# Kernel tuning notes

Hardware: AMD Instinct MI355X
Metric: run time of the kernel (lower is better)

## Reference

```python
import jax, jax.numpy as jnp
import numpy as np

B, T, F_, H1, H2, HEADS = 64, 128, 64, 32, 64, 4
E = H2 * F_  # embed_dim = hidden_dims[-1] * feats = 4096


def conv2d(x, w, b):
    # x: [b,c,H,W], w: [o,c,kh,kw], SAME padding (kernel 3 -> pad 1)
    y = jax.lax.conv_general_dilated(x, w, (1, 1), 'SAME',
                                     dimension_numbers=('NCHW', 'OIHW', 'NCHW'))
    return y + b[None, :, None, None]


def gru_layer(xs, h0, wg, bg, wc, bc):
    # xs: [b,t,c,H,W]; h0: [b,h,H,W]. Standard ConvGRU cell:
    #   r,u = sigmoid(conv([x,h])); cand = tanh(conv([x, r*h]))
    #   h' = (1-u)*h + u*cand
    def step(h, x):
        g = conv2d(jnp.concatenate([x, h], axis=1), wg, bg)
        r, u = jnp.split(jax.nn.sigmoid(g), 2, axis=1)
        cand = jnp.tanh(conv2d(jnp.concatenate([x, r * h], axis=1), wc, bc))
        h_next = (1.0 - u) * h + u * cand
        return h_next, h_next
    hT, ys = jax.lax.scan(step, h0, jnp.swapaxes(xs, 0, 1))
    return jnp.swapaxes(ys, 0, 1), hT  # [b,t,h,H,W], [b,h,H,W]


def mha(q, k, v, w_qkv, b_qkv, w_out, b_out):
    # q: [b,1,E], k/v: [b,t,E]; torch nn.MultiheadAttention (eval, no dropout)
    wq, wk, wv = jnp.split(w_qkv, 3, axis=0)
    bq, bk, bv = jnp.split(b_qkv, 3, axis=0)
    dh = E // HEADS
    def heads(x, w, bb):
        y = x @ w.T + bb
        b_, l_, _ = y.shape
        return y.reshape(b_, l_, HEADS, dh).transpose(0, 2, 1, 3)  # [b,h,l,dh]
    qh, kh, vh = heads(q, wq, bq), heads(k, wk, bk), heads(v, wv, bv)
    scores = jnp.einsum('bhqd,bhkd->bhqk', qh, kh) / jnp.sqrt(jnp.float32(dh))
    attn = jax.nn.softmax(scores, axis=-1)
    ctx = jnp.einsum('bhqk,bhkd->bhqd', attn, vh)
    ctx = ctx.transpose(0, 2, 1, 3).reshape(q.shape[0], q.shape[1], E)
    return ctx @ w_out.T + b_out


def setup_inputs() -> dict:
    key = jax.random.key(0)
    ks = jax.random.split(key, 24)
    s = 0.05
    d = {'x': jax.random.normal(ks[0], (B, T, F_), dtype=jnp.float32)}
    # encoder layer 0: in=1, h=H1; layer 1: in=H1, h=H2
    d['wg_e0'] = jax.random.normal(ks[1], (2 * H1, 1 + H1, 3, 3)) * s
    d['bg_e0'] = jnp.zeros((2 * H1,))
    d['wc_e0'] = jax.random.normal(ks[2], (H1, 1 + H1, 3, 3)) * s
    d['bc_e0'] = jnp.zeros((H1,))
    d['wg_e1'] = jax.random.normal(ks[3], (2 * H2, H1 + H2, 3, 3)) * s
    d['bg_e1'] = jnp.zeros((2 * H2,))
    d['wc_e1'] = jax.random.normal(ks[4], (H2, H1 + H2, 3, 3)) * s
    d['bc_e1'] = jnp.zeros((H2,))
    # decoder: input dim = 2*H2; hidden dims reversed [H2, H1]
    d['wg_d0'] = jax.random.normal(ks[5], (2 * H2, 2 * H2 + H2, 3, 3)) * s
    d['bg_d0'] = jnp.zeros((2 * H2,))
    d['wc_d0'] = jax.random.normal(ks[6], (H2, 2 * H2 + H2, 3, 3)) * s
    d['bc_d0'] = jnp.zeros((H2,))
    d['wg_d1'] = jax.random.normal(ks[7], (2 * H1, H2 + H1, 3, 3)) * s
    d['bg_d1'] = jnp.zeros((2 * H1,))
    d['wc_d1'] = jax.random.normal(ks[8], (H1, H2 + H1, 3, 3)) * s
    d['bc_d1'] = jnp.zeros((H1,))
    d['w_qkv'] = jax.random.normal(ks[9], (3 * E, E)) * (1.0 / np.sqrt(E))
    d['b_qkv'] = jnp.zeros((3 * E,))
    d['w_out'] = jax.random.normal(ks[10], (E, E)) * (1.0 / np.sqrt(E))
    d['b_out'] = jnp.zeros((E,))
    d['w_fin'] = jax.random.normal(ks[11], (1, H1, 1, 1)) * s
    d['b_fin'] = jnp.zeros((1,))
    return d


def reference(x, wg_e0, bg_e0, wc_e0, bc_e0, wg_e1, bg_e1, wc_e1, bc_e1,
              wg_d0, bg_d0, wc_d0, bc_d0, wg_d1, bg_d1, wc_d1, bc_d1,
              w_qkv, b_qkv, w_out, b_out, w_fin, b_fin):
    b, t, f = x.shape
    xr = x.reshape(b, t, 1, f, 1)
    # encoder (2 ConvGRU layers, zero init states)
    y0, h0 = gru_layer(xr, jnp.zeros((b, H1, f, 1), x.dtype), wg_e0, bg_e0, wc_e0, bc_e0)
    y1, h1 = gru_layer(y0, jnp.zeros((b, H2, f, 1), x.dtype), wg_e1, bg_e1, wc_e1, bc_e1)
    # attention bottleneck: query = last hidden, memory = encoder outputs
    query = h1.reshape(b, 1, E)
    memory = y1.reshape(b, t, E)
    context = mha(query, memory, memory, w_qkv, b_qkv, w_out, b_out)  # [b,1,E]
    ctx = context.reshape(b, 1, H2, f, 1)
    dec_in = jnp.concatenate([y1, jnp.broadcast_to(ctx, (b, t, H2, f, 1))], axis=2)
    # decoder init states: encoder last states reversed -> [h1 (H2), h0 (H1)]
    z0, _ = gru_layer(dec_in, h1, wg_d0, bg_d0, wc_d0, bc_d0)
    z1, _ = gru_layer(z0, h0, wg_d1, bg_d1, wc_d1, bc_d1)  # [b,t,H1,f,1]
    # final 1x1 conv applied per timestep == channel contraction
    rec = jnp.einsum('btcfw,oc->btofw', z1, w_fin[:, :, 0, 0]) + b_fin[None, None, :, None, None]
    return rec.reshape(b, t, f)
```

## Files before the change

kernel.cpp:

```cpp
#include <hip/hip_runtime.h>
#include <cstdint>


#define B_  64
#define T_  128
#define TC  32
#define NCH 4

__device__ __forceinline__ float wsum(float v) {
#pragma unroll
  for (int m = 32; m > 0; m >>= 1) v += __shfl_xor(v, m, 64);
  return v;
}
__device__ __forceinline__ float wmaxr(float v) {
#pragma unroll
  for (int m = 32; m > 0; m >>= 1) v = fmaxf(v, __shfl_xor(v, m, 64));
  return v;
}
__device__ __forceinline__ float sigmoidf_(float x) {
  return 1.f / (1.f + __expf(-x));
}
__device__ __forceinline__ float tanhf_(float x) {
  x = fminf(fmaxf(x, -15.f), 15.f);
  float e2 = __expf(2.f * x);
  return (e2 - 1.f) / (e2 + 1.f);
}

struct PackArgs {
  const float* src[16];
  float* dst[16];
  int intot[16];
  int ic0[16];
  int icn[16];
  int oc[16];
};

__global__ __launch_bounds__(256) void pack_all_kernel(PackArgs pa) {
  const int j = blockIdx.y;
  const int icN = pa.icn[j];
  const int total = pa.oc[j] * icN * 3;
  const int i = blockIdx.x * 256 + threadIdx.x;
  if (i >= total) return;
  const int per_oc = icN * 3;
  const int oc = i / per_oc;
  const int rem = i - oc * per_oc;
  const int ic = rem / 3, dk = rem - ic * 3;
  pa.dst[j][i] =
      pa.src[j][((size_t)(oc * pa.intot[j] + pa.ic0[j] + ic) * 3 + dk) * 3 + 1];
}

template <int INC, int OG, int OCC>
__global__ __launch_bounds__(256) void conv_x_kernel(
    const float* __restrict__ seq, int seqC, size_t sB,
    const float* __restrict__ ctx,
    const float* __restrict__ Wgx, const float* __restrict__ Wcx,
    const float* __restrict__ bg, const float* __restrict__ bc,
    float* __restrict__ out) {
  constexpr int OCT = OG + OCC;
  constexpr int NJ = OG / 32;
  constexpr int NJC = OCC / 32;
  const int btl = blockIdx.x;
  const int b = btl >> 5;
  const int tl = btl & 31;
  const int ocg = threadIdx.x >> 3;
  const int f0 = (threadIdx.x & 7) << 3;
  __shared__ float sin_[INC][72];

  for (int idx = threadIdx.x; idx < INC * 72; idx += 256) {
    int ic = idx / 72, ff = idx - ic * 72;
    float v = 0.f;
    if (ff >= 1 && ff <= 64) {
      int fs = ff - 1;
      v = (ic < seqC)
              ? seq[(size_t)b * sB + (size_t)tl * seqC * 64 + ic * 64 + fs]
              : ctx[((size_t)b * (INC - seqC) + (ic - seqC)) * 64 + fs];
    }
    sin_[ic][ff] = v;
  }
  __syncthreads();

  if constexpr (INC >= 4) {
    {
      float acc[NJ][8];
#pragma unroll
      for (int j = 0; j < NJ; ++j) {
        float bb = bg[ocg + 32 * j];
#pragma unroll
        for (int ff = 0; ff < 8; ++ff) acc[j][ff] = bb;
      }
      for (int ic0 = 0; ic0 < INC; ic0 += 4) {
        float hv[4][10];
#pragma unroll
        for (int q = 0; q < 4; ++q) {
          float4 a4 = *(const float4*)&sin_[ic0 + q][f0];
          float4 b4 = *(const float4*)&sin_[ic0 + q][f0 + 4];
          float2 c2 = *(const float2*)&sin_[ic0 + q][f0 + 8];
          hv[q][0] = a4.x; hv[q][1] = a4.y; hv[q][2] = a4.z; hv[q][3] = a4.w;
          hv[q][4] = b4.x; hv[q][5] = b4.y; hv[q][6] = b4.z; hv[q][7] = b4.w;
          hv[q][8] = c2.x; hv[q][9] = c2.y;
        }
#pragma unroll
        for (int j = 0; j < NJ; ++j) {
          const int oc = ocg + 32 * j;
          const float4* w4 = (const float4*)(Wgx + ((size_t)oc * INC + ic0) * 3);
          float4 wa = w4[0], wb = w4[1], wc4 = w4[2];
          const float wt[12] = {wa.x, wa.y, wa.z, wa.w, wb.x, wb.y, wb.z, wb.w,
                                wc4.x, wc4.y, wc4.z, wc4.w};
#pragma unroll
          for (int q = 0; q < 4; ++q) {
            const float w0 = wt[3 * q], w1 = wt[3 * q + 1], w2 = wt[3 * q + 2];
#pragma unroll
            for (int ff = 0; ff < 8; ++ff)
              acc[j][ff] = fmaf(w0, hv[q][ff], fmaf(w1, hv[q][ff + 1], fmaf(w2, hv[q][ff + 2], acc[j][ff])));
          }
        }
      }
#pragma unroll
      for (int j = 0; j < NJ; ++j) {
        float* dst = out + ((size_t)btl * OCT + ocg + 32 * j) * 64 + f0;
        *(float4*)dst = make_float4(acc[j][0], acc[j][1], acc[j][2], acc[j][3]);
        *(float4*)(dst + 4) = make_float4(acc[j][4], acc[j][5], acc[j][6], acc[j][7]);
      }
    }
    {
      float acc[NJC][8];
#pragma unroll
      for (int j = 0; j < NJC; ++j) {
        float bb = bc[ocg + 32 * j];
#pragma unroll
        for (int ff = 0; ff < 8; ++ff) acc[j][ff] = bb;
      }
      for (int ic0 = 0; ic0 < INC; ic0 += 4) {
        float hv[4][10];
#pragma unroll
        for (int q = 0; q < 4; ++q) {
          float4 a4 = *(const float4*)&sin_[ic0 + q][f0];
          float4 b4 = *(const float4*)&sin_[ic0 + q][f0 + 4];
          float2 c2 = *(const float2*)&sin_[ic0 + q][f0 + 8];
          hv[q][0] = a4.x; hv[q][1] = a4.y; hv[q][2] = a4.z; hv[q][3] = a4.w;
          hv[q][4] = b4.x; hv[q][5] = b4.y; hv[q][6] = b4.z; hv[q][7] = b4.w;
          hv[q][8] = c2.x; hv[q][9] = c2.y;
        }
#pragma unroll
        for (int j = 0; j < NJC; ++j) {
          const int oc = ocg + 32 * j;
          const float4* w4 = (const float4*)(Wcx + ((size_t)oc * INC + ic0) * 3);
          float4 wa = w4[0], wb = w4[1], wc4 = w4[2];
          const float wt[12] = {wa.x, wa.y, wa.z, wa.w, wb.x, wb.y, wb.z, wb.w,
                                wc4.x, wc4.y, wc4.z, wc4.w};
#pragma unroll
          for (int q = 0; q < 4; ++q) {
            const float w0 = wt[3 * q], w1 = wt[3 * q + 1], w2 = wt[3 * q + 2];
#pragma unroll
            for (int ff = 0; ff < 8; ++ff)
              acc[j][ff] = fmaf(w0, hv[q][ff], fmaf(w1, hv[q][ff + 1], fmaf(w2, hv[q][ff + 2], acc[j][ff])));
          }
        }
      }
#pragma unroll
      for (int j = 0; j < NJC; ++j) {
        float* dst = out + ((size_t)btl * OCT + OG + ocg + 32 * j) * 64 + f0;
        *(float4*)dst = make_float4(acc[j][0], acc[j][1], acc[j][2], acc[j][3]);
        *(float4*)(dst + 4) = make_float4(acc[j][4], acc[j][5], acc[j][6], acc[j][7]);
      }
    }
  } else {
    float hv[10];
    {
      float4 a4 = *(const float4*)&sin_[0][f0];
      float4 b4 = *(const float4*)&sin_[0][f0 + 4];
      float2 c2 = *(const float2*)&sin_[0][f0 + 8];
      hv[0] = a4.x; hv[1] = a4.y; hv[2] = a4.z; hv[3] = a4.w;
      hv[4] = b4.x; hv[5] = b4.y; hv[6] = b4.z; hv[7] = b4.w;
      hv[8] = c2.x; hv[9] = c2.y;
    }
#pragma unroll
    for (int j = 0; j < NJ; ++j) {
      const int oc = ocg + 32 * j;
      const float w0 = Wgx[oc * 3], w1 = Wgx[oc * 3 + 1], w2 = Wgx[oc * 3 + 2];
      float acc[8];
#pragma unroll
      for (int ff = 0; ff < 8; ++ff)
        acc[ff] = fmaf(w0, hv[ff], fmaf(w1, hv[ff + 1], fmaf(w2, hv[ff + 2], bg[oc])));
      float* dst = out + ((size_t)btl * OCT + oc) * 64 + f0;
      *(float4*)dst = make_float4(acc[0], acc[1], acc[2], acc[3]);
      *(float4*)(dst + 4) = make_float4(acc[4], acc[5], acc[6], acc[7]);
    }
#pragma unroll
    for (int j = 0; j < NJC; ++j) {
      const int oc = ocg + 32 * j;
      const float w0 = Wcx[oc * 3], w1 = Wcx[oc * 3 + 1], w2 = Wcx[oc * 3 + 2];
      float acc[8];
#pragma unroll
      for (int ff = 0; ff < 8; ++ff)
        acc[ff] = fmaf(w0, hv[ff], fmaf(w1, hv[ff + 1], fmaf(w2, hv[ff + 2], bc[oc])));
      float* dst = out + ((size_t)btl * OCT + OG + oc) * 64 + f0;
      *(float4*)dst = make_float4(acc[0], acc[1], acc[2], acc[3]);
      *(float4*)(dst + 4) = make_float4(acc[4], acc[5], acc[6], acc[7]);
    }
  }
}

template <int HC>
__device__ __forceinline__ void gru_body(
    float* smem,
    const float* __restrict__ A,
    const float* __restrict__ Wgh,
    const float* __restrict__ Wch,
    const float* hinit,
    float* __restrict__ Y, size_t yB,
    float* hfinal, int b) {
  constexpr int NR = HC / 32;
  constexpr int OG = 2 * HC;
  constexpr int OCT = 3 * HC;
  float(*Hs)[68] = (float(*)[68])smem;
  float(*Rs)[68] = (float(*)[68])(smem + HC * 68);
  const int tid = threadIdx.x;
  const int ocg = tid >> 4;
  const int f0 = (tid & 15) << 2;
  const int im = (f0 == 0) ? 0 : f0 - 1;
  const bool lo = (f0 == 0), hi = (f0 == 60);

  float hreg[NR][4];
#pragma unroll
  for (int r = 0; r < NR; ++r) {
    const int oc = ocg + 32 * r;
    const float4 v = *(const float4*)(hinit + ((size_t)b * HC + oc) * 64 + f0);
    hreg[r][0] = v.x; hreg[r][1] = v.y; hreg[r][2] = v.z; hreg[r][3] = v.w;
    *(float4*)&Hs[oc][f0] = v;
  }
  __syncthreads();

  for (int tl = 0; tl < TC; ++tl) {
    const float* Abt = A + ((size_t)b * TC + tl) * (OCT * 64);
    float accr[NR][4], accu[NR][4], accc[NR][4];
#pragma unroll
    for (int r = 0; r < NR; ++r) {
      const int oc = ocg + 32 * r;
      const float4 vr = *(const float4*)(Abt + (size_t)oc * 64 + f0);
      const float4 vu = *(const float4*)(Abt + (size_t)(HC + oc) * 64 + f0);
      const float4 vc = *(const float4*)(Abt + (size_t)(OG + oc) * 64 + f0);
      accr[r][0] = vr.x; accr[r][1] = vr.y; accr[r][2] = vr.z; accr[r][3] = vr.w;
      accu[r][0] = vu.x; accu[r][1] = vu.y; accu[r][2] = vu.z; accu[r][3] = vu.w;
      accc[r][0] = vc.x; accc[r][1] = vc.y; accc[r][2] = vc.z; accc[r][3] = vc.w;
    }
#pragma unroll 2
    for (int hc0 = 0; hc0 < HC; hc0 += 4) {
      float hv[4][6];
#pragma unroll
      for (int q = 0; q < 4; ++q) {
        const float4 h4 = *(const float4*)&Hs[hc0 + q][f0];
        const float lf = Hs[hc0 + q][im];
        const float rt = Hs[hc0 + q][f0 + 4];
        hv[q][0] = lo ? 0.f : lf;
        hv[q][1] = h4.x; hv[q][2] = h4.y; hv[q][3] = h4.z; hv[q][4] = h4.w;
        hv[q][5] = hi ? 0.f : rt;
      }
#pragma unroll
      for (int r = 0; r < NR; ++r) {
        {
          const float4* w4 = (const float4*)(Wgh + ((size_t)(ocg + 32 * r) * HC + hc0) * 3);
          const float4 wa = w4[0], wb = w4[1], wc4 = w4[2];
          const float wt[12] = {wa.x, wa.y, wa.z, wa.w, wb.x, wb.y, wb.z, wb.w,
                                wc4.x, wc4.y, wc4.z, wc4.w};
#pragma unroll
          for (int q = 0; q < 4; ++q) {
            const float w0 = wt[3 * q], w1 = wt[3 * q + 1], w2 = wt[3 * q + 2];
#pragma unroll
            for (int ff = 0; ff < 4; ++ff)
              accr[r][ff] = fmaf(w0, hv[q][ff], fmaf(w1, hv[q][ff + 1], fmaf(w2, hv[q][ff + 2], accr[r][ff])));
          }
        }
        {
          const float4* w4 = (const float4*)(Wgh + ((size_t)(HC + ocg + 32 * r) * HC + hc0) * 3);
          const float4 wa = w4[0], wb = w4[1], wc4 = w4[2];
          const float wt[12] = {wa.x, wa.y, wa.z, wa.w, wb.x, wb.y, wb.z, wb.w,
                                wc4.x, wc4.y, wc4.z, wc4.w};
#pragma unroll
          for (int q = 0; q < 4; ++q) {
            const float w0 = wt[3 * q], w1 = wt[3 * q + 1], w2 = wt[3 * q + 2];
#pragma unroll
            for (int ff = 0; ff < 4; ++ff)
              accu[r][ff] = fmaf(w0, hv[q][ff], fmaf(w1, hv[q][ff + 1], fmaf(w2, hv[q][ff + 2], accu[r][ff])));
          }
        }
      }
    }
    float uu[NR][4];
#pragma unroll
    for (int r = 0; r < NR; ++r) {
      float4 rh;
#pragma unroll
      for (int ff = 0; ff < 4; ++ff) {
        uu[r][ff] = sigmoidf_(accu[r][ff]);
        (&rh.x)[ff] = sigmoidf_(accr[r][ff]) * hreg[r][ff];
      }
      *(float4*)&Rs[ocg + 32 * r][f0] = rh;
    }
    __syncthreads();
#pragma unroll 2
    for (int hc0 = 0; hc0 < HC; hc0 += 4) {
      float hv[4][6];
#pragma unroll
      for (int q = 0; q < 4; ++q) {
        const float4 h4 = *(const float4*)&Rs[hc0 + q][f0];
        const float lf = Rs[hc0 + q][im];
        const float rt = Rs[hc0 + q][f0 + 4];
        hv[q][0] = lo ? 0.f : lf;
        hv[q][1] = h4.x; hv[q][2] = h4.y; hv[q][3] = h4.z; hv[q][4] = h4.w;
        hv[q][5] = hi ? 0.f : rt;
      }
#pragma unroll
      for (int r = 0; r < NR; ++r) {
        const float4* w4 = (const float4*)(Wch + ((size_t)(ocg + 32 * r) * HC + hc0) * 3);
        const float4 wa = w4[0], wb = w4[1], wc4 = w4[2];
        const float wt[12] = {wa.x, wa.y, wa.z, wa.w, wb.x, wb.y, wb.z, wb.w,
                              wc4.x, wc4.y, wc4.z, wc4.w};
#pragma unroll
        for (int q = 0; q < 4; ++q) {
          const float w0 = wt[3 * q], w1 = wt[3 * q + 1], w2 = wt[3 * q + 2];
#pragma unroll
          for (int ff = 0; ff < 4; ++ff)
            accc[r][ff] = fmaf(w0, hv[q][ff], fmaf(w1, hv[q][ff + 1], fmaf(w2, hv[q][ff + 2], accc[r][ff])));
        }
      }
    }
#pragma unroll
    for (int r = 0; r < NR; ++r) {
      const int oc = ocg + 32 * r;
      float4 yv;
#pragma unroll
      for (int ff = 0; ff < 4; ++ff) {
        const float cd = tanhf_(accc[r][ff]);
        const float hn = fmaf(uu[r][ff], cd - hreg[r][ff], hreg[r][ff]);
        hreg[r][ff] = hn;
        (&yv.x)[ff] = hn;
      }
      *(float4*)(Y + (size_t)b * yB + (size_t)tl * (HC * 64) + (size_t)oc * 64 + f0) = yv;
      *(float4*)&Hs[oc][f0] = yv;
    }
    __syncthreads();
  }
#pragma unroll
  for (int r = 0; r < NR; ++r) {
    const int oc = ocg + 32 * r;
    *(float4*)(hfinal + ((size_t)b * HC + oc) * 64 + f0) =
        make_float4(hreg[r][0], hreg[r][1], hreg[r][2], hreg[r][3]);
  }
}

template <int HC>
__global__ __launch_bounds__(512) void gru_rec_kernel(
    const float* __restrict__ A, const float* __restrict__ Wgh,
    const float* __restrict__ Wch, const float* hinit,
    float* __restrict__ Y, size_t yB, float* hfinal) {
  __shared__ float smem[2 * HC * 68];
  gru_body<HC>(smem, A, Wgh, Wch, hinit, Y, yB, hfinal, blockIdx.x);
}

struct GruArgs {
  const float* A;
  const float* Wgh;
  const float* Wch;
  const float* hinit;
  float* Y;
  size_t yB;
  float* hfinal;
};

__global__ __launch_bounds__(512) void gru_fused_kernel(GruArgs g64, GruArgs g32) {
  __shared__ float smem[2 * 64 * 68];
  if (blockIdx.x < 64) {
    gru_body<64>(smem, g64.A, g64.Wgh, g64.Wch, g64.hinit, g64.Y, g64.yB,
                 g64.hfinal, blockIdx.x);
  } else {
    gru_body<32>(smem, g32.A, g32.Wgh, g32.Wch, g32.hinit, g32.Y, g32.yB,
                 g32.hfinal, blockIdx.x - 64);
  }
}

template <bool WT>
__global__ __launch_bounds__(256) void gemm64_kernel(
    const float* __restrict__ W, int wrs,
    const float* __restrict__ X, int xrs,
    float* __restrict__ O, int ors,
    const float* __restrict__ bias, int K,
    int ebh, size_t hsW, size_t hsX, size_t hsO, size_t hsB) {
  int eb = blockIdx.x;
  if (ebh > 0) {
    int h = blockIdx.x / ebh;
    eb = blockIdx.x - h * ebh;
    W += h * hsW; X += h * hsX; O += h * hsO;
    if (bias) bias += h * hsB;
  }
  const int e0 = eb * 64;
  __shared__ float Xs[64][68];
  __shared__ float Ws[64][68];
  const int tb4 = (threadIdx.x & 15) << 2;
  const int te4 = (threadIdx.x >> 4) << 2;
  float acc[4][4] = {};
  for (int k0 = 0; k0 < K; k0 += 64) {
    {
      const int row = threadIdx.x >> 2;
      const int kq = (threadIdx.x & 3) << 4;
      const float* src = X + (size_t)row * xrs + k0 + kq;
#pragma unroll
      for (int q = 0; q < 4; ++q) {
        float4 v = *(const float4*)(src + (q << 2));
        Xs[kq + (q << 2) + 0][row] = v.x;
        Xs[kq + (q << 2) + 1][row] = v.y;
        Xs[kq + (q << 2) + 2][row] = v.z;
        Xs[kq + (q << 2) + 3][row] = v.w;
      }
    }
    if (!WT) {
      const int row = threadIdx.x >> 2;
      const int kq = (threadIdx.x & 3) << 4;
      const float* src = W + (size_t)(e0 + row) * wrs + k0 + kq;
#pragma unroll
      for (int q = 0; q < 4; ++q) {
        float4 v = *(const float4*)(src + (q << 2));
        Ws[kq + (q << 2) + 0][row] = v.x;
        Ws[kq + (q << 2) + 1][row] = v.y;
        Ws[kq + (q << 2) + 2][row] = v.z;
        Ws[kq + (q << 2) + 3][row] = v.w;
      }
    } else {
      const int row = threadIdx.x >> 2;
      const int eq = (threadIdx.x & 3) << 4;
      const float* src = W + (size_t)(k0 + row) * wrs + e0 + eq;
#pragma unroll
      for (int q = 0; q < 4; ++q)
        *(float4*)&Ws[row][eq + (q << 2)] = *(const float4*)(src + (q << 2));
    }
    __syncthreads();
#pragma unroll 8
    for (int k = 0; k < 64; ++k) {
      float4 xv = *(const float4*)&Xs[k][tb4];
      float4 wv4 = *(const float4*)&Ws[k][te4];
      const float xb[4] = {xv.x, xv.y, xv.z, xv.w};
      const float we[4] = {wv4.x, wv4.y, wv4.z, wv4.w};
#pragma unroll
      for (int i = 0; i < 4; ++i)
#pragma unroll
        for (int j = 0; j < 4; ++j) acc[i][j] = fmaf(xb[i], we[j], acc[i][j]);
    }
    __syncthreads();
  }
#pragma unroll
  for (int i = 0; i < 4; ++i)
#pragma unroll
    for (int j = 0; j < 4; ++j) {
      float v = acc[i][j];
      if (bias) v += bias[e0 + te4 + j];
      O[(size_t)(tb4 + i) * ors + e0 + te4 + j] = v;
    }
}

__global__ __launch_bounds__(256) void attn_scores_kernel(
    const float* __restrict__ qkh, const float* __restrict__ mem,
    float* __restrict__ scores) {
  const int b = blockIdx.x >> 4;
  const int tt = blockIdx.x & 15;
  const int h = threadIdx.x >> 6;
  const int lane = threadIdx.x & 63;
  const float4* qk4 = (const float4*)(qkh + ((size_t)b * 4 + h) * 4096);
#pragma unroll 2
  for (int ti = 0; ti < 8; ++ti) {
    const int t = tt * 8 + ti;
    const float4* m4 = (const float4*)(mem + ((size_t)b * 128 + t) * 4096);
    float s = 0.f;
    for (int e = lane; e < 1024; e += 64) {
      float4 q = qk4[e], m = m4[e];
      s = fmaf(q.x, m.x, fmaf(q.y, m.y, fmaf(q.z, m.z, fmaf(q.w, m.w, s))));
    }
    s = wsum(s);
    if (lane == 0) scores[((size_t)b * 4 + h) * 128 + t] = s;
  }
}

__global__ __launch_bounds__(256) void attn_softmax_kernel(
    const float* __restrict__ scores, const float* __restrict__ qbuf,
    const float* __restrict__ bqkv, float* __restrict__ attnp) {
  const int b = blockIdx.x;
  const int h = threadIdx.x >> 6;
  const int lane = threadIdx.x & 63;
  const float4* q4 = (const float4*)(qbuf + (size_t)b * 4096 + h * 1024);
  const float4* k4 = (const float4*)(bqkv + 4096 + h * 1024);
  float qb = 0.f;
#pragma unroll
  for (int d = lane; d < 256; d += 64) {
    float4 q = q4[d], k = k4[d];
    qb = fmaf(q.x, k.x, fmaf(q.y, k.y, fmaf(q.z, k.z, fmaf(q.w, k.w, qb))));
  }
  qb = wsum(qb);
  const float* sc = scores + ((size_t)b * 4 + h) * 128;
  float s0 = (sc[lane] + qb) * 0.03125f;
  float s1 = (sc[lane + 64] + qb) * 0.03125f;
  float mx = wmaxr(fmaxf(s0, s1));
  float e0v = __expf(s0 - mx), e1v = __expf(s1 - mx);
  float inv = 1.f / wsum(e0v + e1v);
  attnp[((size_t)b * 4 + h) * 128 + lane] = e0v * inv;
  attnp[((size_t)b * 4 + h) * 128 + lane + 64] = e1v * inv;
}

__global__ __launch_bounds__(256) void attn_wsum_kernel(
    const float* __restrict__ attnp, const float* __restrict__ mem,
    float* __restrict__ wmem) {
  const int b = blockIdx.x >> 4;
  const int eb = blockIdx.x & 15;
  const int e = eb * 256 + threadIdx.x;
  __shared__ float ap[4][128];
  for (int i = threadIdx.x; i < 512; i += 256)
    ap[i >> 7][i & 127] = attnp[(size_t)b * 512 + i];
  __syncthreads();
  float a0 = 0, a1 = 0, a2 = 0, a3 = 0;
  const float* mb = mem + (size_t)b * 128 * 4096 + e;
#pragma unroll 4
  for (int t = 0; t < 128; ++t) {
    float m = mb[(size_t)t * 4096];
    a0 = fmaf(ap[0][t], m, a0);
    a1 = fmaf(ap[1][t], m, a1);
    a2 = fmaf(ap[2][t], m, a2);
    a3 = fmaf(ap[3][t], m, a3);
  }
  wmem[((size_t)b * 4 + 0) * 4096 + e] = a0;
  wmem[((size_t)b * 4 + 1) * 4096 + e] = a1;
  wmem[((size_t)b * 4 + 2) * 4096 + e] = a2;
  wmem[((size_t)b * 4 + 3) * 4096 + e] = a3;
}

__global__ __launch_bounds__(256) void final_kernel(
    const float* __restrict__ z1c,
    const float* __restrict__ wfin, const float* __restrict__ bfin,
    float* __restrict__ out, int tOff) {
  const int idx = blockIdx.x * 256 + threadIdx.x;
  const int f = idx & 63;
  const int tl = (idx >> 6) & 31;
  const int b = idx >> 11;
  const float* zp = z1c + ((size_t)b * TC + tl) * 2048 + f;
  float a = bfin[0];
#pragma unroll
  for (int c = 0; c < 32; ++c) a = fmaf(wfin[c], zp[c * 64], a);
  out[(size_t)b * 8192 + (size_t)(tOff + tl) * 64 + f] = a;
}

extern "C" void kernel_launch(void* const* d_in, const int* in_sizes, int n_in,
                              void* d_out, int out_size, void* d_ws, size_t ws_size,
                              hipStream_t stream) {
  (void)in_sizes; (void)n_in; (void)out_size;
  const float* x     = (const float*)d_in[0];
  const float* wg_e0 = (const float*)d_in[1];
  const float* bg_e0 = (const float*)d_in[2];
  const float* wc_e0 = (const float*)d_in[3];
  const float* bc_e0 = (const float*)d_in[4];
  const float* wg_e1 = (const float*)d_in[5];
  const float* bg_e1 = (const float*)d_in[6];
  const float* wc_e1 = (const float*)d_in[7];
  const float* bc_e1 = (const float*)d_in[8];
  const float* wg_d0 = (const float*)d_in[9];
  const float* bg_d0 = (const float*)d_in[10];
  const float* wc_d0 = (const float*)d_in[11];
  const float* bc_d0 = (const float*)d_in[12];
  const float* wg_d1 = (const float*)d_in[13];
  const float* bg_d1 = (const float*)d_in[14];
  const float* wc_d1 = (const float*)d_in[15];
  const float* bc_d1 = (const float*)d_in[16];
  const float* w_qkv = (const float*)d_in[17];
  const float* b_qkv = (const float*)d_in[18];
  const float* w_out = (const float*)d_in[19];
  const float* b_out = (const float*)d_in[20];
  const float* w_fin = (const float*)d_in[21];
  const float* b_fin = (const float*)d_in[22];
  float* out = (float*)d_out;

  float* WS = (float*)d_ws;
  size_t off = 0;
  auto alloc = [&](size_t n) { float* p = WS + off; off += (n + 63) & ~(size_t)63; return p; };
  float* Amain = alloc((size_t)B_ * TC * 192 * 64);
  float* A96   = alloc((size_t)B_ * TC * 96 * 64);
  float* Y0c  = alloc((size_t)B_ * TC * 32 * 64);
  float* Y1   = alloc((size_t)B_ * T_ * 64 * 64);
  float* Z0p[2] = {alloc((size_t)B_ * TC * 64 * 64), alloc((size_t)B_ * TC * 64 * 64)};
  float* Z1c  = alloc((size_t)B_ * TC * 32 * 64);
  float* He0p[2] = {alloc((size_t)B_ * 32 * 64), alloc((size_t)B_ * 32 * 64)};
  float* He1p[2] = {alloc((size_t)B_ * 64 * 64), alloc((size_t)B_ * 64 * 64)};
  float* Hd0p[2] = {alloc((size_t)B_ * 64 * 64), alloc((size_t)B_ * 64 * 64)};
  float* Hd1p[2] = {alloc((size_t)B_ * 32 * 64), alloc((size_t)B_ * 32 * 64)};
  float* QBUF = alloc((size_t)B_ * 4096);
  float* QKH  = alloc((size_t)B_ * 4 * 4096);
  float* WMEM = alloc((size_t)B_ * 4 * 4096);
  float* CTXB = alloc((size_t)B_ * 4096);
  float* CTXO = alloc((size_t)B_ * 4096);
  float* SCR  = alloc((size_t)B_ * 4 * 128);
  float* ATTN = alloc((size_t)B_ * 4 * 128);
  float* wgx_e0 = alloc(64 * 1 * 3);    float* wgh_e0 = alloc(64 * 32 * 3);
  float* wcx_e0 = alloc(32 * 1 * 3);    float* wch_e0 = alloc(32 * 32 * 3);
  float* wgx_e1 = alloc(128 * 32 * 3);  float* wgh_e1 = alloc(128 * 64 * 3);
  float* wcx_e1 = alloc(64 * 32 * 3);   float* wch_e1 = alloc(64 * 64 * 3);
  float* wgx_d0 = alloc(128 * 128 * 3); float* wgh_d0 = alloc(128 * 64 * 3);
  float* wcx_d0 = alloc(64 * 128 * 3);  float* wch_d0 = alloc(64 * 64 * 3);
  float* wgx_d1 = alloc(64 * 64 * 3);   float* wgh_d1 = alloc(64 * 32 * 3);
  float* wcx_d1 = alloc(32 * 64 * 3);   float* wch_d1 = alloc(32 * 32 * 3);
  if (ws_size < off * sizeof(float)) return;

  {
    PackArgs pa;
    const float* srcs[16] = {wg_e0, wg_e0, wc_e0, wc_e0, wg_e1, wg_e1, wc_e1, wc_e1,
                             wg_d0, wg_d0, wc_d0, wc_d0, wg_d1, wg_d1, wc_d1, wc_d1};
    float* dsts[16] = {wgx_e0, wgh_e0, wcx_e0, wch_e0, wgx_e1, wgh_e1, wcx_e1, wch_e1,
                       wgx_d0, wgh_d0, wcx_d0, wch_d0, wgx_d1, wgh_d1, wcx_d1, wch_d1};
    int intot[16] = {33, 33, 33, 33, 96, 96, 96, 96, 192, 192, 192, 192, 96, 96, 96, 96};
    int ic0[16]   = {0, 1, 0, 1, 0, 32, 0, 32, 0, 128, 0, 128, 0, 64, 0, 64};
    int icn[16]   = {1, 32, 1, 32, 32, 64, 32, 64, 128, 64, 128, 64, 64, 32, 64, 32};
    int occ[16]   = {64, 64, 32, 32, 128, 128, 64, 64, 128, 128, 64, 64, 64, 64, 32, 32};
    for (int j = 0; j < 16; ++j) {
      pa.src[j] = srcs[j]; pa.dst[j] = dsts[j];
      pa.intot[j] = intot[j]; pa.ic0[j] = ic0[j]; pa.icn[j] = icn[j]; pa.oc[j] = occ[j];
    }
    pack_all_kernel<<<dim3(192, 16), 256, 0, stream>>>(pa);
  }

  hipMemsetAsync(He0p[0], 0, (size_t)B_ * 32 * 64 * 4, stream);
  hipMemsetAsync(He1p[0], 0, (size_t)B_ * 64 * 64 * 4, stream);

  auto conv_e0 = [&](int c) {
    conv_x_kernel<1, 64, 32><<<2048, 256, 0, stream>>>(
        x + (size_t)c * TC * 64, 1, (size_t)T_ * 64, nullptr,
        wgx_e0, wcx_e0, bg_e0, bc_e0, A96);
  };
  auto conv_e1 = [&]() {
    conv_x_kernel<32, 128, 64><<<2048, 256, 0, stream>>>(
        Y0c, 32, (size_t)TC * 32 * 64, nullptr,
        wgx_e1, wcx_e1, bg_e1, bc_e1, Amain);
  };

  conv_e0(0);
  gru_rec_kernel<32><<<64, 512, 0, stream>>>(
      A96, wgh_e0, wch_e0, He0p[0], Y0c, (size_t)TC * 2048, He0p[1]);
  conv_e1();
  for (int c = 0; c < NCH; ++c) {
    GruArgs g64 = {Amain, wgh_e1, wch_e1, He1p[c & 1],
                   Y1 + (size_t)c * TC * 4096, (size_t)T_ * 4096, He1p[(c + 1) & 1]};
    if (c < NCH - 1) {
      conv_e0(c + 1);
      GruArgs g32 = {A96, wgh_e0, wch_e0, He0p[(c + 1) & 1],
                     Y0c, (size_t)TC * 2048, He0p[c & 1]};
      gru_fused_kernel<<<128, 512, 0, stream>>>(g64, g32);
      conv_e1();
    } else {
      gru_rec_kernel<64><<<64, 512, 0, stream>>>(
          g64.A, g64.Wgh, g64.Wch, g64.hinit, g64.Y, g64.yB, g64.hfinal);
    }
  }
  float* He0f = He0p[0];
  float* He1f = He1p[0];

  const float* wq = w_qkv;
  const float* wk = w_qkv + (size_t)4096 * 4096;
  const float* wv = w_qkv + (size_t)8192 * 4096;
  gemm64_kernel<false><<<64, 256, 0, stream>>>(wq, 4096, He1f, 4096, QBUF, 4096,
                                               b_qkv, 4096, 0, 0, 0, 0, 0);
  gemm64_kernel<true><<<256, 256, 0, stream>>>(wk, 4096, QBUF, 4096, QKH, 16384,
                                               nullptr, 1024, 64,
                                               (size_t)1024 * 4096, 1024, 4096, 0);
  attn_scores_kernel<<<B_ * 16, 256, 0, stream>>>(QKH, Y1, SCR);
  attn_softmax_kernel<<<B_, 256, 0, stream>>>(SCR, QBUF, b_qkv, ATTN);
  attn_wsum_kernel<<<B_ * 16, 256, 0, stream>>>(ATTN, Y1, WMEM);
  gemm64_kernel<false><<<64, 256, 0, stream>>>(wv, 4096, WMEM, 16384, CTXB, 4096,
                                               b_qkv + 8192, 4096, 16,
                                               (size_t)1024 * 4096, 4096, 1024, 1024);
  gemm64_kernel<false><<<64, 256, 0, stream>>>(w_out, 4096, CTXB, 4096, CTXO, 4096,
                                               b_out, 4096, 0, 0, 0, 0, 0);

  auto conv_d0 = [&](int c) {
    conv_x_kernel<128, 128, 64><<<2048, 256, 0, stream>>>(
        Y1 + (size_t)c * TC * 4096, 64, (size_t)T_ * 4096, CTXO,
        wgx_d0, wcx_d0, bg_d0, bc_d0, Amain);
  };
  auto conv_d1 = [&](int c) {
    conv_x_kernel<64, 64, 32><<<2048, 256, 0, stream>>>(
        Z0p[c & 1], 64, (size_t)TC * 4096, nullptr,
        wgx_d1, wcx_d1, bg_d1, bc_d1, A96);
  };

  conv_d0(0);
  gru_rec_kernel<64><<<64, 512, 0, stream>>>(
      Amain, wgh_d0, wch_d0, He1f, Z0p[0], (size_t)TC * 4096, Hd0p[1]);
  conv_d1(0);
  for (int c = 1; c < NCH; ++c) {
    conv_d0(c);
    GruArgs g64 = {Amain, wgh_d0, wch_d0, Hd0p[c & 1],
                   Z0p[c & 1], (size_t)TC * 4096, Hd0p[(c + 1) & 1]};
    GruArgs g32 = {A96, wgh_d1, wch_d1,
                   (c - 1 == 0 ? He0f : Hd1p[(c - 1) & 1]),
                   Z1c, (size_t)TC * 2048, Hd1p[c & 1]};
    gru_fused_kernel<<<128, 512, 0, stream>>>(g64, g32);
    final_kernel<<<512, 256, 0, stream>>>(Z1c, w_fin, b_fin, out, (c - 1) * TC);
    conv_d1(c);
  }
  gru_rec_kernel<32><<<64, 512, 0, stream>>>(
      A96, wgh_d1, wch_d1, Hd1p[1], Z1c, (size_t)TC * 2048, Hd1p[0]);
  final_kernel<<<512, 256, 0, stream>>>(Z1c, w_fin, b_fin, out, 3 * TC);
}
```

Before: 8.425 ms.

## Overlap decoder conv and final projection with GRU recurrence in one mega-kernel

Adds a mega_kernel that runs the decoder GRU recurrence blocks alongside independent conv_x input projections and final 1x1 projection tiles for other chunks, selected by block index. Double-buffered activation workspaces (Amp, A96p, Z1p) let the next chunk's convolution proceed while the current recurrence runs. The goal is to fill the GPU, which otherwise sits mostly idle during the 64/128-block sequential GRU kernels, and to cut the number of launches. It needs extra workspace, falls back to the old path when that is not available, and the smem size and 512-thread blocks may reduce occupancy for the conv work.

New measurement: 7.721 ms. 1.09x faster.

```diff
diff --git a/kernel.cpp b/kernel.cpp
--- a/kernel.cpp
+++ b/kernel.cpp
@@ -50,7 +50,8 @@
 }
 
 template <int INC, int OG, int OCC>
-__global__ __launch_bounds__(256) void conv_x_kernel(
+__device__ __forceinline__ void conv_x_body(
+    float (*sin_)[72], int tid, int btl,
     const float* __restrict__ seq, int seqC, size_t sB,
     const float* __restrict__ ctx,
     const float* __restrict__ Wgx, const float* __restrict__ Wcx,
@@ -59,14 +60,12 @@
   constexpr int OCT = OG + OCC;
   constexpr int NJ = OG / 32;
   constexpr int NJC = OCC / 32;
-  const int btl = blockIdx.x;
   const int b = btl >> 5;
   const int tl = btl & 31;
-  const int ocg = threadIdx.x >> 3;
-  const int f0 = (threadIdx.x & 7) << 3;
-  __shared__ float sin_[INC][72];
-
-  for (int idx = threadIdx.x; idx < INC * 72; idx += 256) {
+  const int ocg = tid >> 3;
+  const int f0 = (tid & 7) << 3;
+
+  for (int idx = tid; idx < INC * 72; idx += 256) {
     int ic = idx / 72, ff = idx - ic * 72;
     float v = 0.f;
     if (ff >= 1 && ff <= 64) {
@@ -201,15 +200,46 @@
   }
 }
 
+template <int INC, int OG, int OCC>
+__global__ __launch_bounds__(256) void conv_x_kernel(
+    const float* __restrict__ seq, int seqC, size_t sB,
+    const float* __restrict__ ctx,
+    const float* __restrict__ Wgx, const float* __restrict__ Wcx,
+    const float* __restrict__ bg, const float* __restrict__ bc,
+    float* __restrict__ out) {
+  __shared__ float sin_[INC][72];
+  conv_x_body<INC, OG, OCC>(sin_, threadIdx.x, blockIdx.x, seq, seqC, sB, ctx,
+                            Wgx, Wcx, bg, bc, out);
+}
+
+__device__ __forceinline__ void final_body(
+    int tid, int tile, const float* __restrict__ z1c,
+    const float* __restrict__ wfin, const float* __restrict__ bfin,
+    float* __restrict__ out, int tOff) {
+  const int idx = tile * 256 + tid;
+  const int f = idx & 63;
+  const int tl = (idx >> 6) & 31;
+  const int b = idx >> 11;
+  const float* zp = z1c + ((size_t)b * TC + tl) * 2048 + f;
+  float a = bfin[0];
+#pragma unroll
+  for (int c = 0; c < 32; ++c) a = fmaf(wfin[c], zp[c * 64], a);
+  out[(size_t)b * 8192 + (size_t)(tOff + tl) * 64 + f] = a;
+}
+
+__global__ __launch_bounds__(256) void final_kernel(
+    const float* __restrict__ z1c,
+    const float* __restrict__ wfin, const float* __restrict__ bfin,
+    float* __restrict__ out, int tOff) {
+  final_body(threadIdx.x, blockIdx.x, z1c, wfin, bfin, out, tOff);
+}
+
 template <int HC>
 __device__ __forceinline__ void gru_body(
     float* smem,
-    const float* __restrict__ A,
-    const float* __restrict__ Wgh,
-    const float* __restrict__ Wch,
-    const float* hinit,
-    float* __restrict__ Y, size_t yB,
-    float* hfinal, int b) {
+    const float* __restrict__ A, const float* __restrict__ Wgh,
+    const float* __restrict__ Wch, const float* hinit,
+    float* __restrict__ Y, size_t yB, float* hfinal, int b) {
   constexpr int NR = HC / 32;
   constexpr int OG = 2 * HC;
   constexpr int OCT = 3 * HC;
@@ -376,6 +406,67 @@
   } else {
     gru_body<32>(smem, g32.A, g32.Wgh, g32.Wch, g32.hinit, g32.Y, g32.yB,
                  g32.hfinal, blockIdx.x - 64);
+  }
+}
+
+struct ConvJob {
+  int kind;
+  int nblk;
+  const float* seq;
+  int seqC;
+  size_t sB;
+  const float* ctx;
+  const float* w0;
+  const float* w1;
+  const float* b0;
+  const float* b1;
+  float* out;
+  int tOff;
+};
+
+struct MegaArgs {
+  GruArgs g64;
+  GruArgs g32;
+  int ng64, ng32, njobs;
+  ConvJob jobs[4];
+};
+
+__global__ __launch_bounds__(512) void mega_kernel(MegaArgs ma) {
+  __shared__ float smem[18432];
+  int bid = blockIdx.x;
+  if (bid < ma.ng64) {
+    gru_body<64>(smem, ma.g64.A, ma.g64.Wgh, ma.g64.Wch, ma.g64.hinit,
+                 ma.g64.Y, ma.g64.yB, ma.g64.hfinal, bid);
+    return;
+  }
+  bid -= ma.ng64;
+  if (bid < ma.ng32) {
+    gru_body<32>(smem, ma.g32.A, ma.g32.Wgh, ma.g32.Wch, ma.g32.hinit,
+                 ma.g32.Y, ma.g32.yB, ma.g32.hfinal, bid);
+    return;
+  }
+  bid -= ma.ng32;
+  const int half = threadIdx.x >> 8;
+  const int tid = threadIdx.x & 255;
+#pragma unroll 1
+  for (int j = 0; j < ma.njobs; ++j) {
+    if (bid < ma.jobs[j].nblk) {
+      const ConvJob cj = ma.jobs[j];
+      const int tile = bid * 2 + half;
+      if (cj.kind == 2) {
+        conv_x_body<128, 128, 64>((float(*)[72])(smem + half * 128 * 72), tid,
+                                  tile, cj.seq, cj.seqC, cj.sB, cj.ctx, cj.w0,
+                                  cj.w1, cj.b0, cj.b1, cj.out);
+      } else if (cj.kind == 3) {
+        conv_x_body<64, 64, 32>((float(*)[72])(smem + half * 64 * 72), tid,
+                                tile, cj.seq, cj.seqC, cj.sB, cj.ctx, cj.w0,
+                                cj.w1, cj.b0, cj.b1, cj.out);
+      } else {
+        final_body(tid, tile, cj.seq, cj.w0, cj.b0, cj.out, cj.tOff);
+      }
+      return;
+    }
+    bid -= ma.jobs[j].nblk;
   }
 }
 
@@ -528,21 +619,6 @@
   wmem[((size_t)b * 4 + 1) * 4096 + e] = a1;
   wmem[((size_t)b * 4 + 2) * 4096 + e] = a2;
   wmem[((size_t)b * 4 + 3) * 4096 + e] = a3;
-}
-
-__global__ __launch_bounds__(256) void final_kernel(
-    const float* __restrict__ z1c,
-    const float* __restrict__ wfin, const float* __restrict__ bfin,
-    float* __restrict__ out, int tOff) {
-  const int idx = blockIdx.x * 256 + threadIdx.x;
-  const int f = idx & 63;
-  const int tl = (idx >> 6) & 31;
-  const int b = idx >> 11;
-  const float* zp = z1c + ((size_t)b * TC + tl) * 2048 + f;
-  float a = bfin[0];
-#pragma unroll
-  for (int c = 0; c < 32; ++c) a = fmaf(wfin[c], zp[c * 64], a);
-  out[(size_t)b * 8192 + (size_t)(tOff + tl) * 64 + f] = a;
 }
 
 extern "C" void kernel_launch(void* const* d_in, const int* in_sizes, int n_in,
@@ -577,12 +653,12 @@
   float* WS = (float*)d_ws;
   size_t off = 0;
   auto alloc = [&](size_t n) { float* p = WS + off; off += (n + 63) & ~(size_t)63; return p; };
-  float* Amain = alloc((size_t)B_ * TC * 192 * 64);
-  float* A96   = alloc((size_t)B_ * TC * 96 * 64);
+  float* Amp0 = alloc((size_t)B_ * TC * 192 * 64);
+  float* A960 = alloc((size_t)B_ * TC * 96 * 64);
   float* Y0c  = alloc((size_t)B_ * TC * 32 * 64);
   float* Y1   = alloc((size_t)B_ * T_ * 64 * 64);
   float* Z0p[2] = {alloc((size_t)B_ * TC * 64 * 64), alloc((size_t)B_ * TC * 64 * 64)};
-  float* Z1c  = alloc((size_t)B_ * TC * 32 * 64);
+  float* Z1p0 = alloc((size_t)B_ * TC * 32 * 64);
   float* He0p[2] = {alloc((size_t)B_ * 32 * 64), alloc((size_t)B_ * 32 * 64)};
   float* He1p[2] = {alloc((size_t)B_ * 64 * 64), alloc((size_t)B_ * 64 * 64)};
   float* Hd0p[2] = {alloc((size_t)B_ * 64 * 64), alloc((size_t)B_ * 64 * 64)};
@@ -602,7 +678,17 @@
   float* wcx_d0 = alloc(64 * 128 * 3);  float* wch_d0 = alloc(64 * 64 * 3);
   float* wgx_d1 = alloc(64 * 64 * 3);   float* wgh_d1 = alloc(64 * 32 * 3);
   float* wcx_d1 = alloc(32 * 64 * 3);   float* wch_d1 = alloc(32 * 32 * 3);
-  if (ws_size < off * sizeof(float)) return;
+  const size_t off_r9 = off;
+  float* Amp1 = alloc((size_t)B_ * TC * 192 * 64);
+  float* A961 = alloc((size_t)B_ * TC * 96 * 64);
+  float* Z1p1 = alloc((size_t)B_ * TC * 32 * 64);
+  const size_t off_full = off;
+  if (ws_size < off_r9 * sizeof(float)) return;
+  const bool mega_ok = (ws_size >= off_full * sizeof(float));
+
+  float* Amp[2] = {Amp0, Amp1};
+  float* A96p[2] = {A960, A961};
+  float* Z1p[2] = {Z1p0, Z1p1};
 
   {
     PackArgs pa;
@@ -627,24 +713,24 @@
   auto conv_e0 = [&](int c) {
     conv_x_kernel<1, 64, 32><<<2048, 256, 0, stream>>>(
         x + (size_t)c * TC * 64, 1, (size_t)T_ * 64, nullptr,
-        wgx_e0, wcx_e0, bg_e0, bc_e0, A96);
+        wgx_e0, wcx_e0, bg_e0, bc_e0, A96p[0]);
   };
   auto conv_e1 = [&]() {
     conv_x_kernel<32, 128, 64><<<2048, 256, 0, stream>>>(
         Y0c, 32, (size_t)TC * 32 * 64, nullptr,
-        wgx_e1, wcx_e1, bg_e1, bc_e1, Amain);
+        wgx_e1, wcx_e1, bg_e1, bc_e1, Amp[0]);
   };
 
   conv_e0(0);
   gru_rec_kernel<32><<<64, 512, 0, stream>>>(
-      A96, wgh_e0, wch_e0, He0p[0], Y0c, (size_t)TC * 2048, He0p[1]);
+      A96p[0], wgh_e0, wch_e0, He0p[0], Y0c, (size_t)TC * 2048, He0p[1]);
   conv_e1();
   for (int c = 0; c < NCH; ++c) {
-    GruArgs g64 = {Amain, wgh_e1, wch_e1, He1p[c & 1],
+    GruArgs g64 = {Amp[0], wgh_e1, wch_e1, He1p[c & 1],
                    Y1 + (size_t)c * TC * 4096, (size_t)T_ * 4096, He1p[(c + 1) & 1]};
     if (c < NCH - 1) {
       conv_e0(c + 1);
-      GruArgs g32 = {A96, wgh_e0, wch_e0, He0p[(c + 1) & 1],
+      GruArgs g32 = {A96p[0], wgh_e0, wch_e0, He0p[(c + 1) & 1],
                      Y0c, (size_t)TC * 2048, He0p[c & 1]};
       gru_fused_kernel<<<128, 512, 0, stream>>>(g64, g32);
       conv_e1();
@@ -673,33 +759,88 @@
   gemm64_kernel<false><<<64, 256, 0, stream>>>(w_out, 4096, CTXB, 4096, CTXO, 4096,
                                                b_out, 4096, 0, 0, 0, 0, 0);
 
-  auto conv_d0 = [&](int c) {
+  if (mega_ok) {
+    auto JD0 = [&](int c, float* dst) {
+      ConvJob j{}; j.kind = 2; j.nblk = 1024;
+      j.seq = Y1 + (size_t)c * TC * 4096; j.seqC = 64; j.sB = (size_t)T_ * 4096;
+      j.ctx = CTXO; j.w0 = wgx_d0; j.w1 = wcx_d0; j.b0 = bg_d0; j.b1 = bc_d0;
+      j.out = dst; return j;
+    };
+    auto JD1 = [&](float* z0src, float* dst) {
+      ConvJob j{}; j.kind = 3; j.nblk = 1024;
+      j.seq = z0src; j.seqC = 64; j.sB = (size_t)TC * 4096;
+      j.ctx = nullptr; j.w0 = wgx_d1; j.w1 = wcx_d1; j.b0 = bg_d1; j.b1 = bc_d1;
+      j.out = dst; return j;
+    };
+    auto JFIN = [&](float* z1src, int tOff) {
+      ConvJob j{}; j.kind = 4; j.nblk = 256;
+      j.seq = z1src; j.w0 = w_fin; j.b0 = b_fin; j.out = out; j.tOff = tOff;
+      return j;
+    };
+    auto mega = [&](const GruArgs* a64, const GruArgs* a32, int nj,
+                    const ConvJob* js) {
+      MegaArgs ma{};
+      ma.ng64 = a64 ? 64 : 0; if (a64) ma.g64 = *a64;
+      ma.ng32 = a32 ? 64 : 0; if (a32) ma.g32 = *a32;
+      ma.njobs = nj;
+      int grid = ma.ng64 + ma.ng32;
+      for (int i = 0; i < nj; ++i) { ma.jobs[i] = js[i]; grid += js[i].nblk; }
+      mega_kernel<<<grid, 512, 0, stream>>>(ma);
+    };
+
+    GruArgs gd0[4], gd1[4];
+    for (int c = 0; c < 4; ++c) {
+      gd0[c] = {Amp[c & 1], wgh_d0, wch_d0,
+                (c == 0 ? He1f : Hd0p[c & 1]),
+                Z0p[c & 1], (size_t)TC * 4096, Hd0p[(c + 1) & 1]};
+      gd1[c] = {A96p[c & 1], wgh_d1, wch_d1,
+                (c == 0 ? He0f : Hd1p[c & 1]),
+                Z1p[c & 1], (size_t)TC * 2048, Hd1p[(c + 1) & 1]};
+    }
+
     conv_x_kernel<128, 128, 64><<<2048, 256, 0, stream>>>(
-        Y1 + (size_t)c * TC * 4096, 64, (size_t)T_ * 4096, CTXO,
-        wgx_d0, wcx_d0, bg_d0, bc_d0, Amain);
-  };
-  auto conv_d1 = [&](int c) {
-    conv_x_kernel<64, 64, 32><<<2048, 256, 0, stream>>>(
-        Z0p[c & 1], 64, (size_t)TC * 4096, nullptr,
-        wgx_d1, wcx_d1, bg_d1, bc_d1, A96);
-  };
-
-  conv_d0(0);
-  gru_rec_kernel<64><<<64, 512, 0, stream>>>(
-      Amain, wgh_d0, wch_d0, He1f, Z0p[0], (size_t)TC * 4096, Hd0p[1]);
-  conv_d1(0);
-  for (int c = 1; c < NCH; ++c) {
-    conv_d0(c);
-    GruArgs g64 = {Amain, wgh_d0, wch_d0, Hd0p[c & 1],
-                   Z0p[c & 1], (size_t)TC * 4096, Hd0p[(c + 1) & 1]};
-    GruArgs g32 = {A96, wgh_d1, wch_d1,
-                   (c - 1 == 0 ? He0f : Hd1p[(c - 1) & 1]),
-                   Z1c, (size_t)TC * 2048, Hd1p[c & 1]};
-    gru_fused_kernel<<<128, 512, 0, stream>>>(g64, g32);
-    final_kernel<<<512, 256, 0, stream>>>(Z1c, w_fin, b_fin, out, (c - 1) * TC);
-    conv_d1(c);
-  }
-  gru_rec_kernel<32><<<64, 512, 0, stream>>>(
-      A96, wgh_d1, wch_d1, Hd1p[1], Z1c, (size_t)TC * 2048, Hd1p[0]);
-  final_kernel<<<512, 256, 0, stream>>>(Z1c, w_fin, b_fin, out, 3 * TC);
-}
+        Y1, 64, (size_t)T_ * 4096, CTXO, wgx_d0, wcx_d0, bg_d0, bc_d0, Amp[0]);
+    { ConvJob js[1] = {JD0(1, Amp[1])};
+      mega(&gd0[0], nullptr, 1, js); }
+    { ConvJob js[2] = {JD1(Z0p[0], A96p[0]), JD0(2, Amp[0])};
+      mega(&gd0[1], nullptr, 2, js); }
+    { ConvJob js[2] = {JD1(Z0p[1], A96p[1]), JD0(3, Amp[1])};
+      mega(&gd0[2], &gd1[0], 2, js); }
+    { ConvJob js[2] = {JD1(Z0p[0], A96p[0]), JFIN(Z1p[0], 0)};
+      mega(&gd0[3], &gd1[1], 2, js); }
+    { ConvJob js[2] = {JD1(Z0p[1], A96p[1]), JFIN(Z1p[1], TC)};
+      mega(nullptr, &gd1[2], 2, js); }
+    { ConvJob js[1] = {JFIN(Z1p[0], 2 * TC)};
+      mega(nullptr, &gd1[3], 1, js); }
+    final_kernel<<<512, 256, 0, stream>>>(Z1p[1], w_fin, b_fin, out, 3 * TC);
+  } else {
+    auto conv_d0 = [&](int c) {
+      conv_x_kernel<128, 128, 64><<<2048, 256, 0, stream>>>(
+          Y1 + (size_t)c * TC * 4096, 64, (size_t)T_ * 4096, CTXO,
+          wgx_d0, wcx_d0, bg_d0, bc_d0, Amp[0]);
+    };
+    auto conv_d1 = [&](int c) {
+      conv_x_kernel<64, 64, 32><<<2048, 256, 0, stream>>>(
+          Z0p[c & 1], 64, (size_t)TC * 4096, nullptr,
+          wgx_d1, wcx_d1, bg_d1, bc_d1, A96p[0]);
+    };
+    conv_d0(0);
+    gru_rec_kernel<64><<<64, 512, 0, stream>>>(
+        Amp[0], wgh_d0, wch_d0, He1f, Z0p[0], (size_t)TC * 4096, Hd0p[1]);
+    conv_d1(0);
+    for (int c = 1; c < NCH; ++c) {
+      conv_d0(c);
+      GruArgs g64 = {Amp[0], wgh_d0, wch_d0, Hd0p[c & 1],
+                     Z0p[c & 1], (size_t)TC * 4096, Hd0p[(c + 1) & 1]};
+      GruArgs g32 = {A96p[0], wgh_d1, wch_d1,
+                     (c - 1 == 0 ? He0f : Hd1p[(c - 1) & 1]),
+                     Z1p[0], (size_t)TC * 2048, Hd1p[c & 1]};
+      gru_fused_kernel<<<128, 512, 0, stream>>>(g64, g32);
+      final_kernel<<<512, 256, 0, stream>>>(Z1p[0], w_fin, b_fin, out, (c - 1) * TC);
+      conv_d1(c);
+    }
+    gru_rec_kernel<32><<<64, 512, 0, stream>>>(
+        A96p[0], wgh_d1, wch_d1, Hd1p[1], Z1p[0], (size_t)TC * 2048, Hd1p[0]);
+    final_kernel<<<512, 256, 0, stream>>>(Z1p[0], w_fin, b_fin, out, 3 * TC);
+  }
+}
```
